# Kernel optimization log

Hardware: AMD Instinct MI355X
Metric: run time of the kernel (lower is better)

## Reference

```python
import jax, jax.numpy as jnp
import numpy as np
import math
from jax import lax


def quick_gelu(v):
    return v * jax.nn.sigmoid(1.702 * v)


def setup_inputs() -> dict:
    key = jax.random.key(0)
    k0, k1, k2, k3 = jax.random.split(key, 4)
    B, N, C, dim = 64, 1024, 768, 8
    x = jax.random.normal(k0, (B, N, C), dtype=jnp.float32)
    # adapter_down: Linear(C -> dim), xavier-ish init
    Wd = jax.random.normal(k1, (C, dim), dtype=jnp.float32) * (1.0 / math.sqrt(C))
    bd = jnp.zeros((dim,), dtype=jnp.float32)
    # adapter_conv: Conv2d(dim, dim, 3, stride=1, pad=1), HWIO layout
    Wc = jax.random.normal(k2, (3, 3, dim, dim), dtype=jnp.float32) * (1.0 / math.sqrt(9 * dim))
    bc = jnp.zeros((dim,), dtype=jnp.float32)
    # adapter_up: Linear(dim -> C); torch inits this to zeros, but use small
    # random values so the output/gradients are non-trivial for testing.
    Wu = jax.random.normal(k3, (dim, C), dtype=jnp.float32) * 0.02
    bu = jnp.zeros((C,), dtype=jnp.float32)
    return {"x": x, "Wd": Wd, "bd": bd, "Wc": Wc, "bc": bc, "Wu": Wu, "bu": bu}


def reference(x, Wd, bd, Wc, bc, Wu, bu):
    B, N, C = x.shape
    H = int(math.isqrt(N))  # N is a static perfect square (patch grid)
    dim = Wd.shape[1]
    # down projection: [B, N, C] -> [B, N, dim]
    x_down = jnp.einsum("bnc,cd->bnd", x, Wd) + bd
    # reshape to NHWC patch grid, activate, 3x3 same-pad conv
    x_patch = quick_gelu(x_down.reshape(B, H, H, dim))
    x_patch = lax.conv_general_dilated(
        x_patch, Wc, window_strides=(1, 1), padding="SAME",
        dimension_numbers=("NHWC", "HWIO", "NHWC")) + bc
    # flatten back, activate (dropout = identity in eval), up projection
    x_down = quick_gelu(x_patch.reshape(B, N, dim))
    x_up = jnp.einsum("bnd,dc->bnc", x_down, Wu) + bu
    return x_up
```

## Files before the change

### kernel.cpp

```cpp
#include <hip/hip_runtime.h>

#define B_  64
#define N_  1024
#define H_  32
#define C_  768
#define D_  8

#define QCHUNKS    4
#define IMG_PER_Q  (B_ / QCHUNKS)
#define ROWS_PER_Q (IMG_PER_Q * N_)
#define NDOWN      512
#define NCONV      (IMG_PER_Q * 4)
#define NUPB       256

__device__ __forceinline__ float qgelu(float v) {
    return v / (1.0f + __expf(-1.702f * v));
}

typedef float f32x4_t __attribute__((ext_vector_type(4)));
__device__ __forceinline__ float4 ntload4(const float4* p) {
    f32x4_t v = __builtin_nontemporal_load((const f32x4_t*)p);
    return make_float4(v.x, v.y, v.z, v.w);
}
__device__ __forceinline__ void ntstore4(float4 v, float4* p) {
    f32x4_t t; t.x = v.x; t.y = v.y; t.z = v.z; t.w = v.w;
    __builtin_nontemporal_store(t, (f32x4_t*)p);
}

__device__ __forceinline__ void reduce8(float* acc, int lane) {
    {
        const bool hi = lane & 1;
#pragma unroll
        for (int j = 0; j < 4; ++j) {
            const float a = acc[j], b = acc[j + 4];
            acc[j] = hi ? b : a;
            acc[j + 4] = hi ? a : b;
        }
#pragma unroll
        for (int j = 0; j < 4; ++j)
            acc[j] += __shfl_xor(acc[j + 4], 1, 64);
    }
    {
        const bool hi = lane & 2;
#pragma unroll
        for (int j = 0; j < 2; ++j) {
            const float a = acc[j], b = acc[j + 2];
            acc[j] = hi ? b : a;
            acc[j + 2] = hi ? a : b;
        }
#pragma unroll
        for (int j = 0; j < 2; ++j)
            acc[j] += __shfl_xor(acc[j + 2], 2, 64);
    }
    {
        const bool hi = lane & 4;
        const float a = acc[0], b = acc[1];
        acc[0] = hi ? b : a;
        acc[1] = hi ? a : b;
        acc[0] += __shfl_xor(acc[1], 4, 64);
    }
    acc[0] += __shfl_xor(acc[0], 8, 64);
    acc[0] += __shfl_xor(acc[0], 16, 64);
    acc[0] += __shfl_xor(acc[0], 32, 64);
}

__global__ __launch_bounds__(256) void k_step(
    const float* __restrict__ x,  const float* __restrict__ Wd,
    const float* __restrict__ bd, float* __restrict__ t1,
    const float* __restrict__ Wc, const float* __restrict__ bc,
    float* __restrict__ t2,       const float* __restrict__ Wu,
    const float* __restrict__ bu, float* __restrict__ out,
    int nUp, int upC, int nDown, int downC, int nConv, int convC)
{
    __shared__ float smem[D_ * C_];
    const int wid  = threadIdx.x >> 6;
    const int lane = threadIdx.x & 63;
    const int bid  = blockIdx.x;

    if (bid < nUp) {
        float* sW = smem;
        for (int i = threadIdx.x; i < D_ * C_; i += 256) sW[i] = Wu[i];
        __syncthreads();

        float4 ub[3];
#pragma unroll
        for (int j = 0; j < 3; ++j)
            ub[j] = *(const float4*)&bu[(lane + j * 64) * 4];

        const int rowBase = upC * ROWS_PER_Q + bid * 64 + wid * 16;
#pragma unroll 1
        for (int pr = 0; pr < 8; ++pr) {
            const int row = rowBase + pr * 2;
            const float4* rp = (const float4*)(t2 + (size_t)row * D_);
            const float4 r0a = rp[0], r0b = rp[1];
            const float4 r1a = rp[2], r1b = rp[3];
            const float rv0[D_] = { r0a.x,r0a.y,r0a.z,r0a.w, r0b.x,r0b.y,r0b.z,r0b.w };
            const float rv1[D_] = { r1a.x,r1a.y,r1a.z,r1a.w, r1b.x,r1b.y,r1b.z,r1b.w };

            float4 o0[3], o1[3];
#pragma unroll
            for (int j = 0; j < 3; ++j) { o0[j] = ub[j]; o1[j] = ub[j]; }
#pragma unroll
            for (int d = 0; d < D_; ++d) {
#pragma unroll
                for (int j = 0; j < 3; ++j) {
                    const float4 wv = *(const float4*)&sW[d * C_ + (lane + j * 64) * 4];
                    o0[j].x += rv0[d] * wv.x; o0[j].y += rv0[d] * wv.y;
                    o0[j].z += rv0[d] * wv.z; o0[j].w += rv0[d] * wv.w;
                    o1[j].x += rv1[d] * wv.x; o1[j].y += rv1[d] * wv.y;
                    o1[j].z += rv1[d] * wv.z; o1[j].w += rv1[d] * wv.w;
                }
            }
            float* orow0 = out + (size_t)row * C_;
#pragma unroll
            for (int j = 0; j < 3; ++j) {
                ntstore4(o0[j], (float4*)&orow0[(lane + j * 64) * 4]);
                ntstore4(o1[j], (float4*)&orow0[C_ + (lane + j * 64) * 4]);
            }
        }
    } else if (bid < nUp + nDown) {
        float* sW = smem;
        for (int i = threadIdx.x; i < D_ * C_; i += 256) {
            const int c = i >> 3, d = i & 7;
            sW[d * C_ + c] = Wd[i];
        }
        __syncthreads();

        const int dl = 4 * (lane & 1) + 2 * ((lane >> 1) & 1) + ((lane >> 2) & 1);
        const float bias = bd[dl];
        const int pairBase = (downC * ROWS_PER_Q >> 1) + (bid - nUp) * 16 + wid * 4;

#pragma unroll 1
        for (int i = 0; i < 4; ++i) {
            const int p = pairBase + i;
            const float4* x0 = (const float4*)(x + (size_t)(2 * p) * C_);
            const float4* x1 = x0 + (C_ / 4);

            float4 va[3], vb[3];
#pragma unroll
            for (int k = 0; k < 3; ++k) {
                va[k] = ntload4(&x0[k * 64 + lane]);
                vb[k] = ntload4(&x1[k * 64 + lane]);
            }

            float a0[D_], a1[D_];
#pragma unroll
            for (int d = 0; d < D_; ++d) { a0[d] = 0.0f; a1[d] = 0.0f; }

#pragma unroll
            for (int k = 0; k < 3; ++k) {
#pragma unroll
                for (int d = 0; d < D_; ++d) {
                    const float4 wv = *(const float4*)&sW[d * C_ + (k * 64 + lane) * 4];
                    a0[d] += va[k].x * wv.x + va[k].y * wv.y
                           + va[k].z * wv.z + va[k].w * wv.w;
                    a1[d] += vb[k].x * wv.x + vb[k].y * wv.y
                           + vb[k].z * wv.z + vb[k].w * wv.w;
                }
            }
            reduce8(a0, lane);
            reduce8(a1, lane);
            if (lane < 16) {
                const float s = (lane & 8) ? a1[0] : a0[0];
                t1[(size_t)(2 * p + ((lane >> 3) & 1)) * D_ + dl] = qgelu(s + bias);
            }
        }
    } else {
        float* sIn = smem;
        float* sWc = smem + 2560;
        float* sbc = smem + 3136;

        const int idx   = bid - nUp - nDown;
        const int img   = convC * IMG_PER_Q + (idx >> 2);
        const int strip = idx & 3;
        const int h0    = strip * 8;
        const float* in = t1 + (size_t)img * N_ * D_;

#pragma unroll
        for (int j = 0; j < 10; ++j) {
            const int i   = threadIdx.x + j * 256;
            const int lr  = i >> 8;
            const int rem = i & 255;
            const int g   = h0 - 1 + lr;
            sIn[i] = (g >= 0 && g < H_) ? in[(size_t)g * H_ * D_ + rem] : 0.0f;
        }
        for (int i = threadIdx.x; i < 9 * D_ * D_; i += 256) sWc[i] = Wc[i];
        if (threadIdx.x < D_) sbc[threadIdx.x] = bc[threadIdx.x];
        __syncthreads();

        const int lh = threadIdx.x >> 5;
        const int w  = threadIdx.x & 31;
        float acc[D_];
#pragma unroll
        for (int co = 0; co < D_; ++co) acc[co] = sbc[co];
#pragma unroll
        for (int kh = 0; kh < 3; ++kh) {
            const int lrow = lh + kh;
#pragma unroll
            for (int kw = 0; kw < 3; ++kw) {
                const int ww = w + kw - 1;
                if (ww < 0 || ww >= H_) continue;
                const float* ip = &sIn[(lrow * H_ + ww) * D_];
                const float* wp = &sWc[(kh * 3 + kw) * D_ * D_];
#pragma unroll
                for (int ci = 0; ci < D_; ++ci) {
                    const float iv = ip[ci];
#pragma unroll
                    for (int co = 0; co < D_; ++co)
                        acc[co] += iv * wp[ci * D_ + co];
                }
            }
        }
        float4 o0, o1;
        o0.x = qgelu(acc[0]); o0.y = qgelu(acc[1]);
        o0.z = qgelu(acc[2]); o0.w = qgelu(acc[3]);
        o1.x = qgelu(acc[4]); o1.y = qgelu(acc[5]);
        o1.z = qgelu(acc[6]); o1.w = qgelu(acc[7]);
        float* tp = t2 + ((size_t)img * N_ + (size_t)(h0 + lh) * H_ + w) * D_;
        *(float4*)tp       = o0;
        *(float4*)(tp + 4) = o1;
    }
}

extern "C" void kernel_launch(void* const* d_in, const int* in_sizes, int n_in,
                              void* d_out, int out_size, void* d_ws, size_t ws_size,
                              hipStream_t stream) {
    const float* x  = (const float*)d_in[0];
    const float* Wd = (const float*)d_in[1];
    const float* bd = (const float*)d_in[2];
    const float* Wc = (const float*)d_in[3];
    const float* bc = (const float*)d_in[4];
    const float* Wu = (const float*)d_in[5];
    const float* bu = (const float*)d_in[6];
    float* out = (float*)d_out;

    const int nrows = B_ * N_;
    float* t1 = (float*)d_ws;
    float* t2 = t1 + (size_t)nrows * D_;

    for (int s = 0; s < QCHUNKS + 2; ++s) {
        const int nD = (s < QCHUNKS) ? NDOWN : 0;
        const int nC = (s >= 1 && s <= QCHUNKS) ? NCONV : 0;
        const int nU = (s >= 2) ? NUPB : 0;
        k_step<<<nU + nD + nC, 256, 0, stream>>>(
            x, Wd, bd, t1, Wc, bc, t2, Wu, bu, out,
            nU, s - 2, nD, s, nC, s - 1);
    }
}
```

Baseline: 113.9 us.

## Fuse down and up projection work into same 512-thread blocks per step

Rather than launching separate block types for down projection and up projection, each of 512 main blocks now does both in one loop: loading x rows for the down projection and t2 rows for the up projection, then computing each. This interleaves the read-heavy and write-heavy streams inside a block. Blocks grow to 512 threads and conv blocks handle two strips each. Shared memory doubles to hold both weight matrices, which may reduce occupancy. In steps where only one stage is active, half of each block sits idle.

```diff
diff --git a/kernel.cpp b/kernel.cpp
--- a/kernel.cpp
+++ b/kernel.cpp
@@ -9,9 +9,8 @@
 #define QCHUNKS    4
 #define IMG_PER_Q  (B_ / QCHUNKS)
 #define ROWS_PER_Q (IMG_PER_Q * N_)
-#define NDOWN      512
-#define NCONV      (IMG_PER_Q * 4)
-#define NUPB       256
+#define NMAIN      512
+#define NCONVB     32
 
 __device__ __forceinline__ float qgelu(float v) {
     return v / (1.0f + __expf(-1.702f * v));
@@ -64,135 +63,139 @@
     acc[0] += __shfl_xor(acc[0], 32, 64);
 }
 
-__global__ __launch_bounds__(256) void k_step(
+__global__ __launch_bounds__(512) void k_step(
     const float* __restrict__ x,  const float* __restrict__ Wd,
     const float* __restrict__ bd, float* __restrict__ t1,
     const float* __restrict__ Wc, const float* __restrict__ bc,
     float* __restrict__ t2,       const float* __restrict__ Wu,
     const float* __restrict__ bu, float* __restrict__ out,
-    int nUp, int upC, int nDown, int downC, int nConv, int convC)
+    int downC, int upC, int convC)
 {
-    __shared__ float smem[D_ * C_];
-    const int wid  = threadIdx.x >> 6;
-    const int lane = threadIdx.x & 63;
-    const int bid  = blockIdx.x;
-
-    if (bid < nUp) {
-        float* sW = smem;
-        for (int i = threadIdx.x; i < D_ * C_; i += 256) sW[i] = Wu[i];
+    __shared__ float smem[2 * D_ * C_];
+    const int tid = threadIdx.x;
+    const int bid = blockIdx.x;
+
+    if (bid < NMAIN) {
+        float* sWd = smem;
+        float* sWu = smem + D_ * C_;
+        for (int i = tid; i < D_ * C_; i += 512) {
+            const int c = i >> 3, d = i & 7;
+            sWd[d * C_ + c] = Wd[i];
+            sWu[i] = Wu[i];
+        }
         __syncthreads();
+
+        const int wid  = tid >> 6;
+        const int lane = tid & 63;
+        const int dl   = 4 * (lane & 1) + 2 * ((lane >> 1) & 1) + ((lane >> 2) & 1);
+        const float bias = bd[dl];
 
         float4 ub[3];
 #pragma unroll
         for (int j = 0; j < 3; ++j)
             ub[j] = *(const float4*)&bu[(lane + j * 64) * 4];
 
-        const int rowBase = upC * ROWS_PER_Q + bid * 64 + wid * 16;
+        const bool hasD = (downC >= 0);
+        const bool hasU = (upC >= 0);
+        const int drow0 = downC * ROWS_PER_Q + bid * 32 + wid * 4;
+        const int urow0 = upC   * ROWS_PER_Q + bid * 32 + wid * 4;
+
 #pragma unroll 1
-        for (int pr = 0; pr < 8; ++pr) {
-            const int row = rowBase + pr * 2;
-            const float4* rp = (const float4*)(t2 + (size_t)row * D_);
-            const float4 r0a = rp[0], r0b = rp[1];
-            const float4 r1a = rp[2], r1b = rp[3];
-            const float rv0[D_] = { r0a.x,r0a.y,r0a.z,r0a.w, r0b.x,r0b.y,r0b.z,r0b.w };
-            const float rv1[D_] = { r1a.x,r1a.y,r1a.z,r1a.w, r1b.x,r1b.y,r1b.z,r1b.w };
-
-            float4 o0[3], o1[3];
-#pragma unroll
-            for (int j = 0; j < 3; ++j) { o0[j] = ub[j]; o1[j] = ub[j]; }
-#pragma unroll
-            for (int d = 0; d < D_; ++d) {
+        for (int it = 0; it < 2; ++it) {
+            float rv0[D_], rv1[D_];
+            if (hasU) {
+                const float4* rp = (const float4*)(t2 + (size_t)(urow0 + it * 2) * D_);
+                const float4 a = rp[0], b = rp[1], c = rp[2], d = rp[3];
+                rv0[0]=a.x; rv0[1]=a.y; rv0[2]=a.z; rv0[3]=a.w;
+                rv0[4]=b.x; rv0[5]=b.y; rv0[6]=b.z; rv0[7]=b.w;
+                rv1[0]=c.x; rv1[1]=c.y; rv1[2]=c.z; rv1[3]=c.w;
+                rv1[4]=d.x; rv1[5]=d.y; rv1[6]=d.z; rv1[7]=d.w;
+            }
+            float4 va[3], vb[3];
+            if (hasD) {
+                const float4* x0 = (const float4*)(x + (size_t)(drow0 + it * 2) * C_);
+                const float4* x1 = x0 + (C_ / 4);
+#pragma unroll
+                for (int k = 0; k < 3; ++k) {
+                    va[k] = ntload4(&x0[k * 64 + lane]);
+                    vb[k] = ntload4(&x1[k * 64 + lane]);
+                }
+            }
+            if (hasU) {
+                float4 o0[3], o1[3];
+#pragma unroll
+                for (int j = 0; j < 3; ++j) { o0[j] = ub[j]; o1[j] = ub[j]; }
+#pragma unroll
+                for (int d = 0; d < D_; ++d) {
+#pragma unroll
+                    for (int j = 0; j < 3; ++j) {
+                        const float4 wv = *(const float4*)&sWu[d * C_ + (lane + j * 64) * 4];
+                        o0[j].x += rv0[d] * wv.x; o0[j].y += rv0[d] * wv.y;
+                        o0[j].z += rv0[d] * wv.z; o0[j].w += rv0[d] * wv.w;
+                        o1[j].x += rv1[d] * wv.x; o1[j].y += rv1[d] * wv.y;
+                        o1[j].z += rv1[d] * wv.z; o1[j].w += rv1[d] * wv.w;
+                    }
+                }
+                float* orow = out + (size_t)(urow0 + it * 2) * C_;
 #pragma unroll
                 for (int j = 0; j < 3; ++j) {
-                    const float4 wv = *(const float4*)&sW[d * C_ + (lane + j * 64) * 4];
-                    o0[j].x += rv0[d] * wv.x; o0[j].y += rv0[d] * wv.y;
-                    o0[j].z += rv0[d] * wv.z; o0[j].w += rv0[d] * wv.w;
-                    o1[j].x += rv1[d] * wv.x; o1[j].y += rv1[d] * wv.y;
-                    o1[j].z += rv1[d] * wv.z; o1[j].w += rv1[d] * wv.w;
-                }
-            }
-            float* orow0 = out + (size_t)row * C_;
-#pragma unroll
-            for (int j = 0; j < 3; ++j) {
-                ntstore4(o0[j], (float4*)&orow0[(lane + j * 64) * 4]);
-                ntstore4(o1[j], (float4*)&orow0[C_ + (lane + j * 64) * 4]);
-            }
-        }
-    } else if (bid < nUp + nDown) {
-        float* sW = smem;
-        for (int i = threadIdx.x; i < D_ * C_; i += 256) {
-            const int c = i >> 3, d = i & 7;
-            sW[d * C_ + c] = Wd[i];
-        }
-        __syncthreads();
-
-        const int dl = 4 * (lane & 1) + 2 * ((lane >> 1) & 1) + ((lane >> 2) & 1);
-        const float bias = bd[dl];
-        const int pairBase = (downC * ROWS_PER_Q >> 1) + (bid - nUp) * 16 + wid * 4;
-
-#pragma unroll 1
-        for (int i = 0; i < 4; ++i) {
-            const int p = pairBase + i;
-            const float4* x0 = (const float4*)(x + (size_t)(2 * p) * C_);
-            const float4* x1 = x0 + (C_ / 4);
-
-            float4 va[3], vb[3];
-#pragma unroll
-            for (int k = 0; k < 3; ++k) {
-                va[k] = ntload4(&x0[k * 64 + lane]);
-                vb[k] = ntload4(&x1[k * 64 + lane]);
-            }
-
-            float a0[D_], a1[D_];
-#pragma unroll
-            for (int d = 0; d < D_; ++d) { a0[d] = 0.0f; a1[d] = 0.0f; }
-
-#pragma unroll
-            for (int k = 0; k < 3; ++k) {
-#pragma unroll
-                for (int d = 0; d < D_; ++d) {
-                    const float4 wv = *(const float4*)&sW[d * C_ + (k * 64 + lane) * 4];
-                    a0[d] += va[k].x * wv.x + va[k].y * wv.y
-                           + va[k].z * wv.z + va[k].w * wv.w;
-                    a1[d] += vb[k].x * wv.x + vb[k].y * wv.y
-                           + vb[k].z * wv.z + vb[k].w * wv.w;
-                }
-            }
-            reduce8(a0, lane);
-            reduce8(a1, lane);
-            if (lane < 16) {
-                const float s = (lane & 8) ? a1[0] : a0[0];
-                t1[(size_t)(2 * p + ((lane >> 3) & 1)) * D_ + dl] = qgelu(s + bias);
+                    ntstore4(o0[j], (float4*)&orow[(lane + j * 64) * 4]);
+                    ntstore4(o1[j], (float4*)&orow[C_ + (lane + j * 64) * 4]);
+                }
+            }
+            if (hasD) {
+                float a0[D_], a1[D_];
+#pragma unroll
+                for (int d = 0; d < D_; ++d) { a0[d] = 0.0f; a1[d] = 0.0f; }
+#pragma unroll
+                for (int k = 0; k < 3; ++k) {
+#pragma unroll
+                    for (int d = 0; d < D_; ++d) {
+                        const float4 wv = *(const float4*)&sWd[d * C_ + (k * 64 + lane) * 4];
+                        a0[d] += va[k].x * wv.x + va[k].y * wv.y
+                               + va[k].z * wv.z + va[k].w * wv.w;
+                        a1[d] += vb[k].x * wv.x + vb[k].y * wv.y
+                               + vb[k].z * wv.z + vb[k].w * wv.w;
+                    }
+                }
+                reduce8(a0, lane);
+                reduce8(a1, lane);
+                if (lane < 16) {
+                    const float s = (lane & 8) ? a1[0] : a0[0];
+                    t1[(size_t)(drow0 + it * 2 + ((lane >> 3) & 1)) * D_ + dl]
+                        = qgelu(s + bias);
+                }
             }
         }
     } else {
-        float* sIn = smem;
-        float* sWc = smem + 2560;
-        float* sbc = smem + 3136;
-
-        const int idx   = bid - nUp - nDown;
-        const int img   = convC * IMG_PER_Q + (idx >> 2);
+        const int half = tid >> 8;
+        const int tt   = tid & 255;
+        const int idx  = (bid - NMAIN) * 2 + half;
+        const int img  = convC * IMG_PER_Q + (idx >> 2);
         const int strip = idx & 3;
         const int h0    = strip * 8;
         const float* in = t1 + (size_t)img * N_ * D_;
 
+        float* sIn  = smem + half * 3200;
+        float* sWcb = smem + 6400;
+
 #pragma unroll
         for (int j = 0; j < 10; ++j) {
-            const int i   = threadIdx.x + j * 256;
+            const int i   = tt + j * 256;
             const int lr  = i >> 8;
             const int rem = i & 255;
             const int g   = h0 - 1 + lr;
             sIn[i] = (g >= 0 && g < H_) ? in[(size_t)g * H_ * D_ + rem] : 0.0f;
         }
-        for (int i = threadIdx.x; i < 9 * D_ * D_; i += 256) sWc[i] = Wc[i];
-        if (threadIdx.x < D_) sbc[threadIdx.x] = bc[threadIdx.x];
+        for (int i = tid; i < 584; i += 512)
+            sWcb[i] = (i < 576) ? Wc[i] : bc[i - 576];
         __syncthreads();
 
-        const int lh = threadIdx.x >> 5;
-        const int w  = threadIdx.x & 31;
+        const int lh = tt >> 5;
+        const int w  = tt & 31;
         float acc[D_];
 #pragma unroll
-        for (int co = 0; co < D_; ++co) acc[co] = sbc[co];
+        for (int co = 0; co < D_; ++co) acc[co] = sWcb[576 + co];
 #pragma unroll
         for (int kh = 0; kh < 3; ++kh) {
             const int lrow = lh + kh;
@@ -201,7 +204,7 @@
                 const int ww = w + kw - 1;
                 if (ww < 0 || ww >= H_) continue;
                 const float* ip = &sIn[(lrow * H_ + ww) * D_];
-                const float* wp = &sWc[(kh * 3 + kw) * D_ * D_];
+                const float* wp = &sWcb[(kh * 3 + kw) * D_ * D_];
 #pragma unroll
                 for (int ci = 0; ci < D_; ++ci) {
                     const float iv = ip[ci];
@@ -239,11 +242,11 @@
     float* t2 = t1 + (size_t)nrows * D_;
 
     for (int s = 0; s < QCHUNKS + 2; ++s) {
-        const int nD = (s < QCHUNKS) ? NDOWN : 0;
-        const int nC = (s >= 1 && s <= QCHUNKS) ? NCONV : 0;
-        const int nU = (s >= 2) ? NUPB : 0;
-        k_step<<<nU + nD + nC, 256, 0, stream>>>(
-            x, Wd, bd, t1, Wc, bc, t2, Wu, bu, out,
-            nU, s - 2, nD, s, nC, s - 1);
-    }
-}
+        const int downC = (s < QCHUNKS) ? s : -1;
+        const int upC   = (s >= 2) ? s - 2 : -1;
+        const int convC = (s >= 1 && s <= QCHUNKS) ? s - 1 : -1;
+        const int nConv = (convC >= 0) ? NCONVB : 0;
+        k_step<<<NMAIN + nConv, 512, 0, stream>>>(
+            x, Wd, bd, t1, Wc, bc, t2, Wu, bu, out, downC, upC, convC);
+    }
+}
```

New measurement: 123.5 us. +8.4%, slower.
